# Performance work log

Hardware: AMD Instinct MI355X
Metric: run time of the kernel (lower is better)

The kernel has to match this reference:

```python
import jax, jax.numpy as jnp
import numpy as np

N_NODES = 1_000_000
N_EDGES = 32_000_000


def setup_inputs() -> dict:
    key = jax.random.key(0)
    k_x, k_e, k_w1, k_w2 = jax.random.split(key, 4)
    x = jax.random.normal(k_x, (N_NODES, 2), dtype=jnp.float32)
    edge_index = jax.random.randint(k_e, (2, N_EDGES), 0, N_NODES, dtype=jnp.int64)
    # Glorot-ish init for the tiny GCN weights
    W1 = jax.random.normal(k_w1, (2, 8), dtype=jnp.float32) * 0.5
    b1 = jnp.zeros((8,), dtype=jnp.float32)
    W2 = jax.random.normal(k_w2, (8, 1), dtype=jnp.float32) * 0.3
    b2 = jnp.zeros((1,), dtype=jnp.float32)
    return {"x": x, "edge_index": edge_index, "W1": W1, "b1": b1, "W2": W2, "b2": b2}


def _gcn_conv(x, src, dst, norm, W, b, n_nodes):
    # PyG GCNConv: h = x @ W; out[i] = sum_{j->i} norm_e * h[j]; out += b
    h = x @ W                                   # [N, out_dim]
    msg = h[src] * norm[:, None]                # gather over edges (incl. self-loops)
    out = jax.ops.segment_sum(msg, dst, num_segments=n_nodes)
    return out + b


def _norm_and_loops(edge_index, n_nodes, dtype):
    # Add self-loops, compute symmetric normalization deg^{-1/2}[src]*deg^{-1/2}[dst]
    loop = jnp.arange(n_nodes, dtype=edge_index.dtype)
    src = jnp.concatenate([edge_index[0], loop])
    dst = jnp.concatenate([edge_index[1], loop])
    deg = jax.ops.segment_sum(jnp.ones_like(dst, dtype=dtype), dst, num_segments=n_nodes)
    dinv = jnp.where(deg > 0, jax.lax.rsqrt(jnp.maximum(deg, 1.0)), 0.0).astype(dtype)
    norm = dinv[src] * dinv[dst]                # [E + N]
    return src, dst, norm


def reference(x, edge_index, W1, b1, W2, b2):
    n_nodes = x.shape[0]
    src, dst, norm = _norm_and_loops(edge_index, n_nodes, x.dtype)
    h = _gcn_conv(x, src, dst, norm, W1, b1, n_nodes)
    h = jax.nn.relu(h)
    h = _gcn_conv(h, src, dst, norm, W2, b2, n_nodes)
    return jax.nn.sigmoid(h)                    # [N, 1]
```

## Files before the change

### kernel.cpp

```cpp
#include <hip/hip_runtime.h>

#define NN 1000000
#define NE 32000000
#define SCAN_B 256

#define BK_SH 11
#define BK_SZ 2048
#define NB 489
#define GAB 512
#define CHUNK 62500
#define NL (NB * GAB)
#define NBS (NL / SCAN_B)
#define TILE 8192
#define CB 512

typedef int vi4 __attribute__((ext_vector_type(4)));

__global__ void detect_kernel(const int* __restrict__ ei, int* __restrict__ flag) {
    __shared__ int nz;
    if (threadIdx.x == 0) nz = 0;
    __syncthreads();
    int w = ei[2 * threadIdx.x + 1];
    if (w != 0) atomicAdd(&nz, 1);
    __syncthreads();
    if (threadIdx.x == 0) *flag = (nz == 0) ? 1 : 0;
}

__global__ void passA_kernel(const int* __restrict__ ei, int* __restrict__ hist,
                             const int* __restrict__ flagp, int nE) {
    __shared__ int h[NB];
    int t = threadIdx.x;
    for (int b = t; b < NB; b += 512) h[b] = 0;
    __syncthreads();
    int shift = *flagp;
    int start = blockIdx.x * CHUNK;
    int end = min(start + CHUNK, nE);
    if (shift == 0) {
        const int* dstp = ei + nE;
        for (int i = start + (t << 2); i < end; i += 2048) {
            vi4 d = __builtin_nontemporal_load((const vi4*)(dstp + i));
            atomicAdd(&h[d.x >> BK_SH], 1);
            atomicAdd(&h[d.y >> BK_SH], 1);
            atomicAdd(&h[d.z >> BK_SH], 1);
            atomicAdd(&h[d.w >> BK_SH], 1);
        }
    } else {
        const int* dstp = ei + ((size_t)nE << 1);
        for (int i = start + (t << 1); i < end; i += 1024) {
            vi4 d2 = __builtin_nontemporal_load((const vi4*)(dstp + ((size_t)i << 1)));
            atomicAdd(&h[d2.x >> BK_SH], 1);
            atomicAdd(&h[d2.z >> BK_SH], 1);
        }
    }
    __syncthreads();
    for (int b = t; b < NB; b += 512)
        hist[(size_t)b * GAB + blockIdx.x] = h[b];
}

__global__ void scan1_kernel(int* __restrict__ data, int* __restrict__ bsum, int n) {
    __shared__ int sm[SCAN_B];
    int t = threadIdx.x;
    int i = blockIdx.x * SCAN_B + t;
    int v = (i < n) ? data[i] : 0;
    sm[t] = v;
    __syncthreads();
    for (int o = 1; o < SCAN_B; o <<= 1) {
        int a = (t >= o) ? sm[t - o] : 0;
        __syncthreads();
        sm[t] += a;
        __syncthreads();
    }
    if (i < n) data[i] = sm[t] - v;
    if (t == SCAN_B - 1) bsum[blockIdx.x] = sm[t];
}

__global__ void scan2_kernel(int* __restrict__ bsum, int nb) {
    __shared__ int sm[1024];
    int t = threadIdx.x;
    int base = t * 4;
    int v[4];
    int s = 0;
#pragma unroll
    for (int j = 0; j < 4; ++j) {
        v[j] = (base + j < nb) ? bsum[base + j] : 0;
        s += v[j];
    }
    sm[t] = s;
    __syncthreads();
    for (int o = 1; o < 1024; o <<= 1) {
        int a = (t >= o) ? sm[t - o] : 0;
        __syncthreads();
        sm[t] += a;
        __syncthreads();
    }
    int run = sm[t] - s;
#pragma unroll
    for (int j = 0; j < 4; ++j) {
        if (base + j < nb) bsum[base + j] = run;
        run += v[j];
    }
}

__device__ __forceinline__ void tile_scan(int t, int lane, int wid,
                                          int* __restrict__ cnt, int* __restrict__ scn,
                                          int* __restrict__ off, int* __restrict__ wsum) {
    int v = (t < NB) ? cnt[t] : 0;
    int sw = v;
#pragma unroll
    for (int o = 1; o < 64; o <<= 1) {
        int n = __shfl_up(sw, o, 64);
        if (lane >= o) sw += n;
    }
    if (lane == 63) wsum[wid] = sw;
    __syncthreads();
    if (t < 8) {
        int w = wsum[t];
        int iw = w;
#pragma unroll
        for (int o = 1; o < 8; o <<= 1) {
            int n = __shfl_up(iw, o, 8);
            if (t >= o) iw += n;
        }
        wsum[t] = iw - w;
    }
    __syncthreads();
    if (t < NB) { scn[t] = wsum[wid] + sw - v; off[t] = 0; }
    __syncthreads();
}

__global__ void __launch_bounds__(CB, 2)
passC_kernel(const int* __restrict__ ei, const int* __restrict__ hist,
             const int* __restrict__ bsum, unsigned int* __restrict__ pairs,
             const int* __restrict__ flagp, int nE) {
    __shared__ int cnt[NB];
    __shared__ int scn[NB];
    __shared__ int off[NB];
    __shared__ int curb[NB];
    __shared__ int wsum[8];
    __shared__ unsigned int stg[TILE];
    __shared__ unsigned short bkt[TILE];

    int t = threadIdx.x;
    int lane = t & 63, wid = t >> 6;
    for (int b = t; b < NB; b += CB) {
        int flat = b * GAB + blockIdx.x;
        curb[b] = hist[flat] + bsum[flat >> 8];
        cnt[b] = 0;
    }
    __syncthreads();
    int shift = *flagp;
    int start = blockIdx.x * CHUNK;
    int end = min(start + CHUNK, nE);

    if (shift == 1) {
        const size_t dbase = (size_t)nE << 1;
        for (int ts = start; ts < end; ts += TILE) {
            int te = min(ts + TILE, end);
            int tn = te - ts;
            vi4 dd[8];
#pragma unroll
            for (int q = 0; q < 8; ++q) {
                int i = ts + (t << 1) + (q << 10);
                if (i + 2 <= te) {
                    dd[q] = __builtin_nontemporal_load(
                        (const vi4*)(ei + dbase + ((size_t)i << 1)));
                    atomicAdd(&cnt[dd[q].x >> BK_SH], 1);
                    atomicAdd(&cnt[dd[q].z >> BK_SH], 1);
                }
            }
            __syncthreads();
            tile_scan(t, lane, wid, cnt, scn, off, wsum);
#pragma unroll
            for (int q = 0; q < 8; ++q) {
                int i = ts + (t << 1) + (q << 10);
                if (i + 2 <= te) {
                    vi4 ss = __builtin_nontemporal_load(
                        (const vi4*)(ei + ((size_t)i << 1)));
                    int b0 = dd[q].x >> BK_SH;
                    int pos = scn[b0] + atomicAdd(&off[b0], 1);
                    stg[pos] = (unsigned)ss.x | ((unsigned)(dd[q].x & (BK_SZ - 1)) << 20);
                    bkt[pos] = (unsigned short)b0;
                    int b1 = dd[q].z >> BK_SH;
                    pos = scn[b1] + atomicAdd(&off[b1], 1);
                    stg[pos] = (unsigned)ss.z | ((unsigned)(dd[q].z & (BK_SZ - 1)) << 20);
                    bkt[pos] = (unsigned short)b1;
                }
            }
            __syncthreads();
            for (int j = t; j < tn; j += CB) {
                int b = bkt[j];
                pairs[curb[b] + (j - scn[b])] = stg[j];
            }
            __syncthreads();
            for (int b = t; b < NB; b += CB) { curb[b] += cnt[b]; cnt[b] = 0; }
            __syncthreads();
        }
    } else {
        const int* srcp = ei;
        const int* dstp = ei + nE;
        for (int ts = start; ts < end; ts += TILE) {
            int te = min(ts + TILE, end);
            int tn = te - ts;
            vi4 dd[4];
#pragma unroll
            for (int q = 0; q < 4; ++q) {
                int i = ts + (t << 2) + (q << 11);
                if (i + 4 <= te) {
                    dd[q] = __builtin_nontemporal_load((const vi4*)(dstp + i));
                    atomicAdd(&cnt[dd[q].x >> BK_SH], 1);
                    atomicAdd(&cnt[dd[q].y >> BK_SH], 1);
                    atomicAdd(&cnt[dd[q].z >> BK_SH], 1);
                    atomicAdd(&cnt[dd[q].w >> BK_SH], 1);
                }
            }
            __syncthreads();
            tile_scan(t, lane, wid, cnt, scn, off, wsum);
#pragma unroll
            for (int q = 0; q < 4; ++q) {
                int i = ts + (t << 2) + (q << 11);
                if (i + 4 <= te) {
                    vi4 ss = __builtin_nontemporal_load((const vi4*)(srcp + i));
                    int dv[4] = {dd[q].x, dd[q].y, dd[q].z, dd[q].w};
                    int sv[4] = {ss.x, ss.y, ss.z, ss.w};
#pragma unroll
                    for (int e = 0; e < 4; ++e) {
                        int b = dv[e] >> BK_SH;
                        int pos = scn[b] + atomicAdd(&off[b], 1);
                        stg[pos] = (unsigned)sv[e] | ((unsigned)(dv[e] & (BK_SZ - 1)) << 20);
                        bkt[pos] = (unsigned short)b;
                    }
                }
            }
            __syncthreads();
            for (int j = t; j < tn; j += CB) {
                int b = bkt[j];
                pairs[curb[b] + (j - scn[b])] = stg[j];
            }
            __syncthreads();
            for (int b = t; b < NB; b += CB) { curb[b] += cnt[b]; cnt[b] = 0; }
            __syncthreads();
        }
    }
}

__device__ __forceinline__ void bucket_range(const int* __restrict__ hist,
                                             const int* __restrict__ bsum,
                                             int b, int nE, int& base, int& endp) {
    int f0 = b * GAB;
    base = hist[f0] + bsum[f0 >> 8];
    if (b + 1 < NB) {
        int f1 = (b + 1) * GAB;
        endp = hist[f1] + bsum[f1 >> 8];
    } else {
        endp = nE;
    }
}

__device__ __forceinline__ void aligned_range(int base, int endp, int& abase, int& rend) {
    abase = (base + 3) & ~3;
    if (abase > endp) abase = endp;
    rend = abase + ((endp - abase) & ~3);
}

__global__ void passD0_kernel(const unsigned int* __restrict__ pairs,
                              const int* __restrict__ hist, const int* __restrict__ bsum,
                              const float2* __restrict__ x,
                              float* __restrict__ dinv, float2* __restrict__ xd,
                              int nE, int nN) {
    __shared__ int degl[BK_SZ];
    int t = threadIdx.x;
    int b = blockIdx.x;
    for (int j = t; j < BK_SZ; j += 1024) degl[j] = 0;
    __syncthreads();
    int base, endp, abase, rend;
    bucket_range(hist, bsum, b, nE, base, endp);
    aligned_range(base, endp, abase, rend);
    {
        int k = base + t;
        if (k < abase) atomicAdd(&degl[pairs[k] >> 20], 1);
        int k2 = rend + t;
        if (k2 < endp) atomicAdd(&degl[pairs[k2] >> 20], 1);
    }
    for (int k = abase + (t << 2); k + 4 <= rend; k += 4096) {
        vi4 q = *(const vi4*)(pairs + k);
        atomicAdd(&degl[(unsigned)q.x >> 20], 1);
        atomicAdd(&degl[(unsigned)q.y >> 20], 1);
        atomicAdd(&degl[(unsigned)q.z >> 20], 1);
        atomicAdd(&degl[(unsigned)q.w >> 20], 1);
    }
    __syncthreads();
    for (int j = t; j < BK_SZ; j += 1024) {
        int nid = (b << BK_SH) + j;
        if (nid < nN) {
            float di = rsqrtf((float)(degl[j] + 1));
            dinv[nid] = di;
            float2 v = x[nid];
            xd[nid] = make_float2(v.x * di, v.y * di);
        }
    }
}

__global__ void passL1_kernel(const unsigned int* __restrict__ pairs,
                              const int* __restrict__ hist, const int* __restrict__ bsum,
                              const float* __restrict__ dinv, const float2* __restrict__ xd,
                              const float* __restrict__ W1, const float* __restrict__ b1,
                              const float* __restrict__ W2,
                              float* __restrict__ hd, int nE, int nN) {
    __shared__ float ax[BK_SZ];
    __shared__ float ay[BK_SZ];
    int t = threadIdx.x;
    int b = blockIdx.x;
    for (int j = t; j < BK_SZ; j += 1024) { ax[j] = 0.f; ay[j] = 0.f; }
    __syncthreads();
    int base, endp, abase, rend;
    bucket_range(hist, bsum, b, nE, base, endp);
    aligned_range(base, endp, abase, rend);
    {
        int k = base + t;
        if (k < abase) {
            unsigned int p = pairs[k];
            float2 v = xd[p & 0xFFFFF];
            atomicAdd(&ax[p >> 20], v.x);
            atomicAdd(&ay[p >> 20], v.y);
        }
        int k2 = rend + t;
        if (k2 < endp) {
            unsigned int p = pairs[k2];
            float2 v = xd[p & 0xFFFFF];
            atomicAdd(&ax[p >> 20], v.x);
            atomicAdd(&ay[p >> 20], v.y);
        }
    }
    for (int k = abase + (t << 2); k + 4 <= rend; k += 4096) {
        vi4 q = *(const vi4*)(pairs + k);
        unsigned int p[4] = {(unsigned)q.x, (unsigned)q.y, (unsigned)q.z, (unsigned)q.w};
        float2 v[4];
#pragma unroll
        for (int j = 0; j < 4; ++j) v[j] = xd[p[j] & 0xFFFFF];
#pragma unroll
        for (int j = 0; j < 4; ++j) {
            int dl = p[j] >> 20;
            atomicAdd(&ax[dl], v[j].x);
            atomicAdd(&ay[dl], v[j].y);
        }
    }
    __syncthreads();
    for (int j = t; j < BK_SZ; j += 1024) {
        int nid = (b << BK_SH) + j;
        if (nid < nN) {
            float dd = dinv[nid];
            float2 xs = xd[nid];
            float AX = (ax[j] + xs.x * dd) * dd;
            float AY = (ay[j] + xs.y * dd) * dd;
            float acc = 0.f;
#pragma unroll
            for (int c = 0; c < 8; ++c) {
                float h = fmaf(AX, W1[c], fmaf(AY, W1[8 + c], b1[c]));
                acc = fmaf(fmaxf(h, 0.f), W2[c], acc);
            }
            hd[nid] = acc * dd;
        }
    }
}

__global__ void passL2_kernel(const unsigned int* __restrict__ pairs,
                              const int* __restrict__ hist, const int* __restrict__ bsum,
                              const float* __restrict__ dinv, const float* __restrict__ hd,
                              const float* __restrict__ b2,
                              float* __restrict__ out, int nE, int nN) {
    __shared__ float ag[BK_SZ];
    int t = threadIdx.x;
    int b = blockIdx.x;
    for (int j = t; j < BK_SZ; j += 1024) ag[j] = 0.f;
    __syncthreads();
    int base, endp, abase, rend;
    bucket_range(hist, bsum, b, nE, base, endp);
    aligned_range(base, endp, abase, rend);
    {
        int k = base + t;
        if (k < abase) {
            unsigned int p = pairs[k];
            atomicAdd(&ag[p >> 20], hd[p & 0xFFFFF]);
        }
        int k2 = rend + t;
        if (k2 < endp) {
            unsigned int p = pairs[k2];
            atomicAdd(&ag[p >> 20], hd[p & 0xFFFFF]);
        }
    }
    for (int k = abase + (t << 2); k + 4 <= rend; k += 4096) {
        vi4 q = *(const vi4*)(pairs + k);
        unsigned int p[4] = {(unsigned)q.x, (unsigned)q.y, (unsigned)q.z, (unsigned)q.w};
        float v[4];
#pragma unroll
        for (int j = 0; j < 4; ++j) v[j] = hd[p[j] & 0xFFFFF];
#pragma unroll
        for (int j = 0; j < 4; ++j) atomicAdd(&ag[p[j] >> 20], v[j]);
    }
    __syncthreads();
    for (int j = t; j < BK_SZ; j += 1024) {
        int nid = (b << BK_SH) + j;
        if (nid < nN) {
            float z = fmaf(dinv[nid], ag[j] + hd[nid], b2[0]);
            out[nid] = 1.f / (1.f + expf(-z));
        }
    }
}


__global__ void deg_kernel(const int* __restrict__ ei, int* __restrict__ deg,
                           const int* __restrict__ flagp, int nE) {
    int i = blockIdx.x * blockDim.x + threadIdx.x;
    if (i >= nE) return;
    int shift = *flagp;
    int d = ei[((size_t)nE << shift) + ((size_t)i << shift)];
    atomicAdd(&deg[d], 1);
}

__global__ void prep_kernel(const int* __restrict__ deg, const float2* __restrict__ x,
                            float* __restrict__ dinv, float2* __restrict__ xd, int nN) {
    int i = blockIdx.x * blockDim.x + threadIdx.x;
    if (i >= nN) return;
    float di = rsqrtf((float)(deg[i] + 1));
    dinv[i] = di;
    float2 v = x[i];
    xd[i] = make_float2(v.x * di, v.y * di);
}

__device__ __forceinline__ void load_edge(const int* __restrict__ ei, int shift,
                                          int nE, int i, int& s, int& d) {
    s = ei[(size_t)i << shift];
    d = ei[((size_t)nE << shift) + ((size_t)i << shift)];
}

__global__ void l1a_kernel(const int* __restrict__ ei, const float2* __restrict__ xd,
                           float* __restrict__ agg, const int* __restrict__ flagp, int nE) {
    int i = blockIdx.x * blockDim.x + threadIdx.x;
    if (i >= nE) return;
    int shift = *flagp;
    int s, d;
    load_edge(ei, shift, nE, i, s, d);
    float2 v = xd[s];
    unsafeAtomicAdd(&agg[(size_t)d * 2], v.x);
    unsafeAtomicAdd(&agg[(size_t)d * 2 + 1], v.y);
}

__global__ void h2f_kernel(const float2* __restrict__ agg, const float2* __restrict__ xd,
                           const float* __restrict__ dinv, const float* __restrict__ W1,
                           const float* __restrict__ b1, const float* __restrict__ W2,
                           float* __restrict__ hd, int nN) {
    int d = blockIdx.x * blockDim.x + threadIdx.x;
    if (d >= nN) return;
    float dd = dinv[d];
    float2 a = agg[d];
    float2 xs = xd[d];
    float ax = (a.x + xs.x * dd) * dd;
    float ay = (a.y + xs.y * dd) * dd;
    float acc = 0.f;
#pragma unroll
    for (int j = 0; j < 8; ++j) {
        float h = fmaf(ax, W1[j], fmaf(ay, W1[8 + j], b1[j]));
        acc = fmaf(fmaxf(h, 0.f), W2[j], acc);
    }
    hd[d] = acc * dd;
}

__global__ void l2a_kernel(const int* __restrict__ ei, const float* __restrict__ hd,
                           float* __restrict__ out2, const int* __restrict__ flagp, int nE) {
    int i = blockIdx.x * blockDim.x + threadIdx.x;
    if (i >= nE) return;
    int shift = *flagp;
    int s, d;
    load_edge(ei, shift, nE, i, s, d);
    unsafeAtomicAdd(&out2[d], hd[s]);
}

__global__ void finf_kernel(const float* __restrict__ out2, const float* __restrict__ hd,
                            const float* __restrict__ dinv, const float* __restrict__ b2,
                            float* __restrict__ out, int nN) {
    int d = blockIdx.x * blockDim.x + threadIdx.x;
    if (d >= nN) return;
    float z = fmaf(dinv[d], out2[d] + hd[d], b2[0]);
    out[d] = 1.f / (1.f + expf(-z));
}

extern "C" void kernel_launch(void* const* d_in, const int* in_sizes, int n_in,
                              void* d_out, int out_size, void* d_ws, size_t ws_size,
                              hipStream_t stream) {
    const float* x  = (const float*)d_in[0];
    const int*   ei = (const int*)d_in[1];
    const float* W1 = (const float*)d_in[2];
    const float* b1 = (const float*)d_in[3];
    const float* W2 = (const float*)d_in[4];
    const float* b2 = (const float*)d_in[5];
    float* out = (float*)d_out;

    const int nE = NE, nN = NN;
    const int bs = 256;
    char* ws = (char*)d_ws;
    const size_t MiB = 1 << 20;

    const size_t csr_need = 18 * MiB + (size_t)nE * 4;

    if (ws_size >= csr_need) {
        int*          hist  = (int*)ws;
        int*          bsum  = (int*)(ws + 1 * MiB);
        int*          flag  = (int*)(ws + 1 * MiB + 65536);
        float*        dinv  = (float*)(ws + 2 * MiB);
        float2*       xd    = (float2*)(ws + 6 * MiB);
        float*        hd    = (float*)(ws + 14 * MiB);
        unsigned int* pairs = (unsigned int*)(ws + 18 * MiB);

        detect_kernel<<<1, 256, 0, stream>>>(ei, flag);
        passA_kernel<<<GAB, 512, 0, stream>>>(ei, hist, flag, nE);
        scan1_kernel<<<NBS, SCAN_B, 0, stream>>>(hist, bsum, NL);
        scan2_kernel<<<1, 1024, 0, stream>>>(bsum, NBS);
        passC_kernel<<<GAB, CB, 0, stream>>>(ei, hist, bsum, pairs, flag, nE);
        passD0_kernel<<<NB, 1024, 0, stream>>>(pairs, hist, bsum, (const float2*)x,
                                               dinv, xd, nE, nN);
        passL1_kernel<<<NB, 1024, 0, stream>>>(pairs, hist, bsum, dinv, xd,
                                               W1, b1, W2, hd, nE, nN);
        passL2_kernel<<<NB, 1024, 0, stream>>>(pairs, hist, bsum, dinv, hd,
                                               b2, out, nE, nN);
    } else {
        int*    deg  = (int*)ws;
        float*  agg  = (float*)(ws + 4 * MiB);
        float*  out2 = (float*)(ws + 12 * MiB);
        float*  dinv = (float*)(ws + 16 * MiB);
        float2* xd   = (float2*)(ws + 20 * MiB);
        float*  hd   = (float*)(ws + 28 * MiB);
        int*    flag = (int*)(ws + 32 * MiB);

        hipMemsetAsync(ws, 0, 16 * MiB, stream);

        detect_kernel<<<1, 256, 0, stream>>>(ei, flag);
        deg_kernel<<<(nE + bs - 1) / bs, bs, 0, stream>>>(ei, deg, flag, nE);
        prep_kernel<<<(nN + bs - 1) / bs, bs, 0, stream>>>(deg, (const float2*)x, dinv, xd, nN);
        l1a_kernel<<<(nE + bs - 1) / bs, bs, 0, stream>>>(ei, xd, agg, flag, nE);
        h2f_kernel<<<(nN + bs - 1) / bs, bs, 0, stream>>>((const float2*)agg, xd, dinv,
                                                          W1, b1, W2, hd, nN);
        l2a_kernel<<<(nE + bs - 1) / bs, bs, 0, stream>>>(ei, hd, out2, flag, nE);
        finf_kernel<<<(nN + bs - 1) / bs, bs, 0, stream>>>(out2, hd, dinv, b2, out, nN);
    }
}
```

Measured before the change: 997.4 us.

## Add second-level sort by source slice for shared-memory gathers in GCN layers

Adds a new path that re-sorts the destination-bucketed edge list a second time. Within groups of eight destination buckets, edges are ordered by source slice, so both aggregation layers can stage source features for one slice in shared memory and accumulate destinations in a shared-memory tile instead of gathering randomly from global memory. Degree counting moves into the new histogram pass. The cost is an extra full read and write of the edge array, more kernels and scans, and a much larger workspace, with a fallback to the old path when the workspace is too small.

```diff
diff --git a/kernel.cpp b/kernel.cpp
--- a/kernel.cpp
+++ b/kernel.cpp
@@ -13,6 +13,15 @@
 #define NBS (NL / SCAN_B)
 #define TILE 8192
 #define CB 512
+
+#define G8 8
+#define NG 62
+#define NS NB
+#define CHK 8
+#define NL2 (NG * NS * CHK)
+#define NBS2 ((NL2 + SCAN_B - 1) / SCAN_B)
+#define TILE2 16384
+#define SPLIT 4
 
 typedef int vi4 __attribute__((ext_vector_type(4)));
 
@@ -243,17 +252,18 @@
     }
 }
 
+__device__ __forceinline__ int bstart(const int* __restrict__ hist,
+                                      const int* __restrict__ bsum, int b, int nE) {
+    if (b >= NB) return nE;
+    int f = b * GAB;
+    return hist[f] + bsum[f >> 8];
+}
+
 __device__ __forceinline__ void bucket_range(const int* __restrict__ hist,
                                              const int* __restrict__ bsum,
                                              int b, int nE, int& base, int& endp) {
-    int f0 = b * GAB;
-    base = hist[f0] + bsum[f0 >> 8];
-    if (b + 1 < NB) {
-        int f1 = (b + 1) * GAB;
-        endp = hist[f1] + bsum[f1 >> 8];
-    } else {
-        endp = nE;
-    }
+    base = bstart(hist, bsum, b, nE);
+    endp = bstart(hist, bsum, b + 1, nE);
 }
 
 __device__ __forceinline__ void aligned_range(int base, int endp, int& abase, int& rend) {
@@ -404,6 +414,188 @@
             float z = fmaf(dinv[nid], ag[j] + hd[nid], b2[0]);
             out[nid] = 1.f / (1.f + expf(-z));
         }
+    }
+}
+
+
+__global__ void __launch_bounds__(512, 2)
+passBA_kernel(const unsigned int* __restrict__ pairs, const int* __restrict__ hist,
+              const int* __restrict__ bsum, int* __restrict__ hist2,
+              int* __restrict__ deg, int nE, int nN) {
+    __shared__ int h[NS];
+    __shared__ int degl[G8 * BK_SZ];
+    int t = threadIdx.x;
+    int g = blockIdx.x / CHK, c = blockIdx.x % CHK;
+    for (int s = t; s < NS; s += 512) h[s] = 0;
+    for (int j = t; j < G8 * BK_SZ; j += 512) degl[j] = 0;
+    int bn[8];
+#pragma unroll
+    for (int j = 0; j < 8; ++j) bn[j] = bstart(hist, bsum, g * G8 + j, nE);
+    int gb1 = bstart(hist, bsum, (g + 1) * G8, nE);
+    __syncthreads();
+    long long gsz = gb1 - bn[0];
+    int cs = bn[0] + (int)(gsz * c / CHK);
+    int ce = bn[0] + (int)(gsz * (c + 1) / CHK);
+    for (int k = cs + t; k < ce; k += 512) {
+        unsigned int e = pairs[k];
+        atomicAdd(&h[(e & 0xFFFFFu) >> 11], 1);
+        int bg = 0;
+#pragma unroll
+        for (int j = 1; j < 8; ++j) bg += (k >= bn[j]);
+        atomicAdd(&degl[(bg << 11) | (int)(e >> 20)], 1);
+    }
+    __syncthreads();
+    for (int s = t; s < NS; s += 512)
+        hist2[(g * NS + s) * CHK + c] = h[s];
+    for (int j = t; j < G8 * BK_SZ; j += 512) {
+        int dc = degl[j];
+        int node = (g << 14) + j;
+        if (dc && node < nN) atomicAdd(&deg[node], dc);
+    }
+}
+
+__global__ void __launch_bounds__(512, 1)
+passBC_kernel(const unsigned int* __restrict__ pairs, const int* __restrict__ hist,
+              const int* __restrict__ bsum, const int* __restrict__ hist2,
+              const int* __restrict__ bsum2, unsigned int* __restrict__ pairs2, int nE) {
+    __shared__ int cnt[NS];
+    __shared__ int scn[NS];
+    __shared__ int off[NS];
+    __shared__ int curb[NS];
+    __shared__ int wsum[8];
+    __shared__ unsigned int stg[TILE2];
+    __shared__ unsigned short bkt[TILE2];
+    int t = threadIdx.x, lane = t & 63, wid = t >> 6;
+    int g = blockIdx.x / CHK, c = blockIdx.x % CHK;
+    for (int s = t; s < NS; s += 512) {
+        int flat = (g * NS + s) * CHK + c;
+        curb[s] = hist2[flat] + bsum2[flat >> 8];
+        cnt[s] = 0;
+    }
+    int bn[8];
+#pragma unroll
+    for (int j = 0; j < 8; ++j) bn[j] = bstart(hist, bsum, g * G8 + j, nE);
+    int gb1 = bstart(hist, bsum, (g + 1) * G8, nE);
+    __syncthreads();
+    long long gsz = gb1 - bn[0];
+    int cs = bn[0] + (int)(gsz * c / CHK);
+    int ce = bn[0] + (int)(gsz * (c + 1) / CHK);
+    for (int ts = cs; ts < ce; ts += TILE2) {
+        int te = min(ts + TILE2, ce);
+        int tn = te - ts;
+        for (int k = ts + t; k < te; k += 512) {
+            unsigned int e = pairs[k];
+            atomicAdd(&cnt[(e & 0xFFFFFu) >> 11], 1);
+        }
+        __syncthreads();
+        tile_scan(t, lane, wid, cnt, scn, off, wsum);
+        for (int k = ts + t; k < te; k += 512) {
+            unsigned int e = pairs[k];
+            unsigned int src = e & 0xFFFFFu;
+            int ss = src >> 11;
+            int bg = 0;
+#pragma unroll
+            for (int j = 1; j < 8; ++j) bg += (k >= bn[j]);
+            int pos = scn[ss] + atomicAdd(&off[ss], 1);
+            stg[pos] = (src & 2047u) | ((e >> 20) << 11) | ((unsigned)bg << 22);
+            bkt[pos] = (unsigned short)ss;
+        }
+        __syncthreads();
+        for (int j = t; j < tn; j += 512) {
+            int s = bkt[j];
+            pairs2[curb[s] + (j - scn[s])] = stg[j];
+        }
+        __syncthreads();
+        for (int s = t; s < NS; s += 512) { curb[s] += cnt[s]; cnt[s] = 0; }
+        __syncthreads();
+    }
+}
+
+__device__ __forceinline__ void slice_range(const int* __restrict__ hist2,
+                                            const int* __restrict__ bsum2,
+                                            int g, int ss, int nE, int& s0, int& s1) {
+    int f0 = (g * NS + ss) * CHK;
+    s0 = hist2[f0] + bsum2[f0 >> 8];
+    if (ss + 1 < NS) {
+        int f1 = (g * NS + ss + 1) * CHK;
+        s1 = hist2[f1] + bsum2[f1 >> 8];
+    } else if (g + 1 < NG) {
+        int f1 = ((g + 1) * NS) * CHK;
+        s1 = hist2[f1] + bsum2[f1 >> 8];
+    } else {
+        s1 = nE;
+    }
+}
+
+__global__ void passL1g_kernel(const unsigned int* __restrict__ pairs2,
+                               const int* __restrict__ hist2, const int* __restrict__ bsum2,
+                               const float2* __restrict__ xd, float* __restrict__ agg,
+                               int nE, int nN) {
+    __shared__ float2 axy[G8 * BK_SZ];
+    __shared__ float2 xdl[BK_SZ];
+    int t = threadIdx.x;
+    int g = blockIdx.x / SPLIT, sub = blockIdx.x % SPLIT;
+    for (int j = t; j < G8 * BK_SZ; j += 1024) axy[j] = make_float2(0.f, 0.f);
+    __syncthreads();
+    for (int ss = sub; ss < NS; ss += SPLIT) {
+        int bn0 = ss << 11;
+        for (int j = t; j < BK_SZ; j += 1024) {
+            int nid = bn0 + j;
+            xdl[j] = (nid < nN) ? xd[nid] : make_float2(0.f, 0.f);
+        }
+        __syncthreads();
+        int s0, s1;
+        slice_range(hist2, bsum2, g, ss, nE, s0, s1);
+        for (int k = s0 + t; k < s1; k += 1024) {
+            unsigned int e = pairs2[k];
+            float2 v = xdl[e & 2047u];
+            int a = (int)((e >> 22) << 11) | (int)((e >> 11) & 2047u);
+            atomicAdd(&axy[a].x, v.x);
+            atomicAdd(&axy[a].y, v.y);
+        }
+        __syncthreads();
+    }
+    for (int j = t; j < G8 * BK_SZ; j += 1024) {
+        float2 v = axy[j];
+        int node = (g << 14) + j;
+        if ((v.x != 0.f || v.y != 0.f) && node < nN) {
+            unsafeAtomicAdd(&agg[2 * node], v.x);
+            unsafeAtomicAdd(&agg[2 * node + 1], v.y);
+        }
+    }
+}
+
+__global__ void passL2g_kernel(const unsigned int* __restrict__ pairs2,
+                               const int* __restrict__ hist2, const int* __restrict__ bsum2,
+                               const float* __restrict__ hd, float* __restrict__ agg2,
+                               int nE, int nN) {
+    __shared__ float ag[G8 * BK_SZ];
+    __shared__ float hdl[BK_SZ];
+    int t = threadIdx.x;
+    int g = blockIdx.x / SPLIT, sub = blockIdx.x % SPLIT;
+    for (int j = t; j < G8 * BK_SZ; j += 1024) ag[j] = 0.f;
+    __syncthreads();
+    for (int ss = sub; ss < NS; ss += SPLIT) {
+        int bn0 = ss << 11;
+        for (int j = t; j < BK_SZ; j += 1024) {
+            int nid = bn0 + j;
+            hdl[j] = (nid < nN) ? hd[nid] : 0.f;
+        }
+        __syncthreads();
+        int s0, s1;
+        slice_range(hist2, bsum2, g, ss, nE, s0, s1);
+        for (int k = s0 + t; k < s1; k += 1024) {
+            unsigned int e = pairs2[k];
+            float v = hdl[e & 2047u];
+            int a = (int)((e >> 22) << 11) | (int)((e >> 11) & 2047u);
+            atomicAdd(&ag[a], v);
+        }
+        __syncthreads();
+    }
+    for (int j = t; j < G8 * BK_SZ; j += 1024) {
+        float v = ag[j];
+        int node = (g << 14) + j;
+        if (v != 0.f && node < nN) unsafeAtomicAdd(&agg2[node], v);
     }
 }
 
@@ -501,8 +693,42 @@
     const size_t MiB = 1 << 20;
 
     const size_t csr_need = 18 * MiB + (size_t)nE * 4;
-
-    if (ws_size >= csr_need) {
+    const size_t need3 = 160 * MiB + (size_t)nE * 4;
+
+    if (ws_size >= need3) {
+        int*          hist   = (int*)ws;
+        int*          bsum   = (int*)(ws + 1 * MiB);
+        int*          flag   = (int*)(ws + 1 * MiB + 65536);
+        int*          hist2  = (int*)(ws + 2 * MiB);
+        int*          bsum2  = (int*)(ws + 3 * MiB);
+        float*        dinv   = (float*)(ws + 4 * MiB);
+        float2*       xd     = (float2*)(ws + 8 * MiB);
+        float*        hd     = (float*)(ws + 16 * MiB);
+        float*        agg    = (float*)(ws + 20 * MiB);
+        int*          deg    = (int*)(ws + 28 * MiB);
+        unsigned int* pairs  = (unsigned int*)(ws + 32 * MiB);
+        unsigned int* pairs2 = (unsigned int*)(ws + 160 * MiB);
+
+        detect_kernel<<<1, 256, 0, stream>>>(ei, flag);
+        passA_kernel<<<GAB, 512, 0, stream>>>(ei, hist, flag, nE);
+        scan1_kernel<<<NBS, SCAN_B, 0, stream>>>(hist, bsum, NL);
+        scan2_kernel<<<1, 1024, 0, stream>>>(bsum, NBS);
+        passC_kernel<<<GAB, CB, 0, stream>>>(ei, hist, bsum, pairs, flag, nE);
+        hipMemsetAsync(deg, 0, (size_t)nN * 4, stream);
+        passBA_kernel<<<NG * CHK, 512, 0, stream>>>(pairs, hist, bsum, hist2, deg, nE, nN);
+        scan1_kernel<<<NBS2, SCAN_B, 0, stream>>>(hist2, bsum2, NL2);
+        scan2_kernel<<<1, 1024, 0, stream>>>(bsum2, NBS2);
+        prep_kernel<<<(nN + bs - 1) / bs, bs, 0, stream>>>(deg, (const float2*)x, dinv, xd, nN);
+        passBC_kernel<<<NG * CHK, 512, 0, stream>>>(pairs, hist, bsum, hist2, bsum2,
+                                                    pairs2, nE);
+        hipMemsetAsync(agg, 0, (size_t)nN * 8, stream);
+        passL1g_kernel<<<NG * SPLIT, 1024, 0, stream>>>(pairs2, hist2, bsum2, xd, agg, nE, nN);
+        h2f_kernel<<<(nN + bs - 1) / bs, bs, 0, stream>>>((const float2*)agg, xd, dinv,
+                                                          W1, b1, W2, hd, nN);
+        hipMemsetAsync(agg, 0, (size_t)nN * 4, stream);
+        passL2g_kernel<<<NG * SPLIT, 1024, 0, stream>>>(pairs2, hist2, bsum2, hd, agg, nE, nN);
+        finf_kernel<<<(nN + bs - 1) / bs, bs, 0, stream>>>(agg, hd, dinv, b2, out, nN);
+    } else if (ws_size >= csr_need) {
         int*          hist  = (int*)ws;
         int*          bsum  = (int*)(ws + 1 * MiB);
         int*          flag  = (int*)(ws + 1 * MiB + 65536);
```

New measurement: 1.538 ms. 1.54x slower.
